# Kernel optimization log

Measured on AMD Instinct MI355X. Metric: run time of the kernel, lower is better.

Reference implementation:

```python
import jax, jax.numpy as jnp
import numpy as np

NUM_EXPERTS = 3
NUM_CLASSES = 10
HIDDEN = 256


def setup_inputs() -> dict:
    key = jax.random.key(0)
    k_in, k_w1, k_b1, k_w2, k_b2 = jax.random.split(key, 5)
    E, B, C, H, W = NUM_EXPERTS, 8, NUM_CLASSES, 512, 512
    inputs = jax.random.normal(k_in, (E, B, C, H, W), dtype=jnp.float32)
    fan_in1 = E * C
    w1 = jax.random.uniform(k_w1, (fan_in1, HIDDEN), jnp.float32, -1, 1) / np.sqrt(fan_in1)
    b1 = jax.random.uniform(k_b1, (HIDDEN,), jnp.float32, -1, 1) / np.sqrt(fan_in1)
    w2 = jax.random.uniform(k_w2, (HIDDEN, E), jnp.float32, -1, 1) / np.sqrt(HIDDEN)
    b2 = jax.random.uniform(k_b2, (E,), jnp.float32, -1, 1) / np.sqrt(HIDDEN)
    return {"inputs": inputs, "w1": w1, "b1": b1, "w2": w2, "b2": b2}


def reference(inputs, w1, b1, w2, b2):
    # inputs: [E, B, C, H, W] stacked expert logits
    E, B, C, H, W = inputs.shape
    N = B * H * W
    head_logits = jnp.moveaxis(inputs, 2, 1).reshape(E, C, N)   # [E, C, N]
    x = head_logits.reshape(E * C, N).T                          # [N, E*C]
    h = jax.nn.relu(x @ w1 + b1)                                 # [N, HIDDEN]
    exp_logits = h @ w2 + b2                                     # [N, E]
    # softmax is monotonic -> argmax of softmax == argmax of logits
    exp_selected = jnp.argmax(exp_logits, axis=-1)               # [N] int
    # gather the selected expert's logits per pixel (replaces one-hot mult-sum)
    out = head_logits[exp_selected, :, jnp.arange(N)]            # [N, C]
    output = out.T.reshape(C, B, H, W)                           # [C, B, H, W]
    output = jnp.moveaxis(output, 1, 0)                          # [B, C, H, W]
    return output, exp_selected.reshape(B, H, W)
```

## Files before the change

kernel.cpp:

```cpp
#include <hip/hip_runtime.h>

#define HWQ   262144
#define CHW   2621440
#define BCHW  20971520
#define NTOT  2097152

#define NBLOCKS 1024
#define BITERS  8

typedef __attribute__((ext_vector_type(8))) short short8;
typedef __attribute__((ext_vector_type(4))) float f32x4;

union Frag { uint u[4]; uint4 u4; short8 s; };

__device__ __forceinline__ uint bf16w(float x) {
    const uint u = __float_as_uint(x);
    return (u + 0x7FFFu + ((u >> 16) & 1u)) >> 16;
}

__device__ __forceinline__ void split_pair(float a, float b,
                                           uint& h, uint& m, uint& l) {
    const uint ha = bf16w(a), hb = bf16w(b);
    h = ha | (hb << 16);
    const float fa = __uint_as_float(ha << 16);
    const float fb = __uint_as_float(hb << 16);
    const float ra = a - fa, rb = b - fb;
    const uint ma = bf16w(ra), mb = bf16w(rb);
    m = ma | (mb << 16);
    const float ga = __uint_as_float(ma << 16);
    const float gb = __uint_as_float(mb << 16);
    l = bf16w(ra - ga) | (bf16w(rb - gb) << 16);
}

__global__ __launch_bounds__(512)
void mlp_select_mfma(const float* __restrict__ inputs,
                     const float* __restrict__ w1,
                     const float* __restrict__ b1,
                     const float* __restrict__ w2,
                     const float* __restrict__ b2,
                     float* __restrict__ out0,
                     float* __restrict__ out1) {
    __shared__ uint4 Bfrag[16 * 3 * 64];
    __shared__ float W2s[768];
    __shared__ float Logb[8 * 96];

    const int tid = threadIdx.x;

    for (int idx = tid; idx < 16 * 64; idx += 512) {
        const int ht = idx >> 6, ln = idx & 63;
        const int col = (ht << 4) | (ln & 15);
        const int kbs = (ln >> 4) << 3;
        Frag fh, fm, fl;
        #pragma unroll
        for (int jj = 0; jj < 4; ++jj) {
            const int k0 = kbs + 2 * jj, k1 = k0 + 1;
            const float a = (k0 < 30) ? w1[k0 * 256 + col]
                                      : ((k0 == 30) ? b1[col] : 0.f);
            const float b = (k1 < 30) ? w1[k1 * 256 + col]
                                      : ((k1 == 30) ? b1[col] : 0.f);
            split_pair(a, b, fh.u[jj], fm.u[jj], fl.u[jj]);
        }
        const int base = ht * 3 * 64 + ln;
        Bfrag[base]       = fh.u4;
        Bfrag[base + 64]  = fm.u4;
        Bfrag[base + 128] = fl.u4;
    }
    for (int i = tid; i < 768; i += 512) W2s[i] = w2[i];
    __syncthreads();

    const int lane = tid & 63;
    const int wid  = tid >> 6;
    const int l15  = lane & 15;
    const int lg   = lane >> 4;
    const int kb   = lg << 3;

    uint koff[8];
    #pragma unroll
    for (int j = 0; j < 8; ++j) {
        const int k = kb + j;
        const int e = (k >= 20) ? 2 : ((k >= 10) ? 1 : 0);
        const int c = k - e * 10;
        koff[j] = (k < 30) ? (uint)((e * BCHW + c * HWQ) * 4) : 0u;
    }
    const float b20 = b2[0], b21 = b2[1], b22 = b2[2];
    const char* ib = (const char*)inputs;
    char* ob = (char*)out0;

    #pragma unroll 1
    for (int it = 0; it < BITERS; ++it) {
        const int n0 = (blockIdx.x * BITERS + it) * 256 + wid * 32;
        const uint sbase = (uint)((n0 >> 18) * CHW + (n0 & (HWQ - 1))) * 4u;

        short8 Ah[2], Am[2], Al[2];
        #pragma unroll
        for (int t = 0; t < 2; ++t) {
            const uint vb = sbase + (uint)((t * 16 + l15) * 4);
            float xv[8];
            #pragma unroll
            for (int j = 0; j < 8; ++j)
                xv[j] = *(const float*)(ib + (size_t)(vb + koff[j]));
            if (kb == 24) { xv[6] = 1.f; xv[7] = 0.f; }
            Frag ch_, cm_, cl_;
            #pragma unroll
            for (int jj = 0; jj < 4; ++jj)
                split_pair(xv[2 * jj], xv[2 * jj + 1],
                           ch_.u[jj], cm_.u[jj], cl_.u[jj]);
            Ah[t] = ch_.s; Am[t] = cm_.s; Al[t] = cl_.s;
        }

        float lacc[2][4][3];
        #pragma unroll
        for (int t = 0; t < 2; ++t)
            #pragma unroll
            for (int r = 0; r < 4; ++r)
                lacc[t][r][0] = lacc[t][r][1] = lacc[t][r][2] = 0.f;

        #pragma unroll 4
        for (int ht = 0; ht < 16; ++ht) {
            const uint4* bp = &Bfrag[ht * 3 * 64 + lane];
            Frag bh, bm, bl;
            bh.u4 = bp[0]; bm.u4 = bp[64]; bl.u4 = bp[128];
            const int wcol = ((ht << 4) | l15) * 3;
            const float w20 = W2s[wcol], w21 = W2s[wcol + 1], w22 = W2s[wcol + 2];
            #pragma unroll
            for (int t = 0; t < 2; ++t) {
                f32x4 D = {0.f, 0.f, 0.f, 0.f};
                D = __builtin_amdgcn_mfma_f32_16x16x32_bf16(Al[t], bh.s, D, 0, 0, 0);
                D = __builtin_amdgcn_mfma_f32_16x16x32_bf16(Ah[t], bl.s, D, 0, 0, 0);
                D = __builtin_amdgcn_mfma_f32_16x16x32_bf16(Am[t], bm.s, D, 0, 0, 0);
                D = __builtin_amdgcn_mfma_f32_16x16x32_bf16(Am[t], bh.s, D, 0, 0, 0);
                D = __builtin_amdgcn_mfma_f32_16x16x32_bf16(Ah[t], bm.s, D, 0, 0, 0);
                D = __builtin_amdgcn_mfma_f32_16x16x32_bf16(Ah[t], bh.s, D, 0, 0, 0);
                #pragma unroll
                for (int r = 0; r < 4; ++r) {
                    const float hre = fmaxf(D[r], 0.f);
                    lacc[t][r][0] = fmaf(hre, w20, lacc[t][r][0]);
                    lacc[t][r][1] = fmaf(hre, w21, lacc[t][r][1]);
                    lacc[t][r][2] = fmaf(hre, w22, lacc[t][r][2]);
                }
            }
        }

        #pragma unroll
        for (int t = 0; t < 2; ++t)
            #pragma unroll
            for (int r = 0; r < 4; ++r)
                #pragma unroll
                for (int e = 0; e < 3; ++e) {
                    float v = lacc[t][r][e];
                    v += __shfl_xor(v, 1);
                    v += __shfl_xor(v, 2);
                    v += __shfl_xor(v, 4);
                    v += __shfl_xor(v, 8);
                    lacc[t][r][e] = v;
                }

        if (l15 == 0) {
            float* lb = &Logb[wid * 96];
            #pragma unroll
            for (int t = 0; t < 2; ++t)
                #pragma unroll
                for (int r = 0; r < 4; ++r) {
                    const int tk = t * 16 + lg * 4 + r;
                    lb[tk * 3 + 0] = lacc[t][r][0];
                    lb[tk * 3 + 1] = lacc[t][r][1];
                    lb[tk * 3 + 2] = lacc[t][r][2];
                }
        }
        __threadfence_block();

        const int tt = lane & 31;
        const float* lb = &Logb[wid * 96 + tt * 3];
        const float L0 = lb[0] + b20;
        const float L1 = lb[1] + b21;
        const float L2 = lb[2] + b22;
        int sel = 0; float best = L0;
        if (L1 > best) { best = L1; sel = 1; }
        if (L2 > best) { sel = 2; }

        const uint obase = sbase + (uint)(tt * 4);
        const uint ioff  = obase + (uint)sel * (uint)(BCHW * 4);
        const int chalf  = lane >> 5;
        #pragma unroll
        for (int cc = 0; cc < 5; ++cc) {
            const uint cofs = (uint)((chalf * 5 + cc) * (HWQ * 4));
            const float v = *(const float*)(ib + (size_t)(ioff + cofs));
            *(float*)(ob + (size_t)(obase + cofs)) = v;
        }
        if (lane < 32) out1[n0 + tt] = (float)sel;
    }
}

extern "C" void kernel_launch(void* const* d_in, const int* in_sizes, int n_in,
                              void* d_out, int out_size, void* d_ws, size_t ws_size,
                              hipStream_t stream) {
    const float* inputs = (const float*)d_in[0];
    const float* w1     = (const float*)d_in[1];
    const float* b1     = (const float*)d_in[2];
    const float* w2     = (const float*)d_in[3];
    const float* b2     = (const float*)d_in[4];

    float* out0 = (float*)d_out;
    float* out1 = out0 + BCHW;

    mlp_select_mfma<<<NBLOCKS, 512, 0, stream>>>(
        inputs, w1, b1, w2, b2, out0, out1);
}
```

Baseline: 496.4 us.

## Use persistent 768-block grid, occupancy hint, and shuffle-based argmax

Reduces the grid to 768 blocks that stride over 8192 work tiles, so each block handles about 11 tiles, and adds a launch-bounds occupancy hint of 6. The per-wave LDS logit buffer and its fence are replaced by computing the argmax in registers after the xor reduction, packing the selections into a word and redistributing it with a single shuffle. The b2 bias is folded into the accumulator initialisation, pre-scaled by 1/16 because the 16-lane reduction sums it back. The occupancy bound may force register spilling, and the last pass over the tiles leaves some blocks idle.

```diff
diff --git a/kernel.cpp b/kernel.cpp
--- a/kernel.cpp
+++ b/kernel.cpp
@@ -5,8 +5,9 @@
 #define BCHW  20971520
 #define NTOT  2097152
 
-#define NBLOCKS 1024
-#define BITERS  8
+#define NBLOCKS   768
+#define NBLKITER  8192
+#define BITERS    11
 
 typedef __attribute__((ext_vector_type(8))) short short8;
 typedef __attribute__((ext_vector_type(4))) float f32x4;
@@ -32,7 +33,7 @@
     l = bf16w(ra - ga) | (bf16w(rb - gb) << 16);
 }
 
-__global__ __launch_bounds__(512)
+__global__ __launch_bounds__(512, 6)
 void mlp_select_mfma(const float* __restrict__ inputs,
                      const float* __restrict__ w1,
                      const float* __restrict__ b1,
@@ -42,7 +43,6 @@
                      float* __restrict__ out1) {
     __shared__ uint4 Bfrag[16 * 3 * 64];
     __shared__ float W2s[768];
-    __shared__ float Logb[8 * 96];
 
     const int tid = threadIdx.x;
 
@@ -82,13 +82,15 @@
         const int c = k - e * 10;
         koff[j] = (k < 30) ? (uint)((e * BCHW + c * HWQ) * 4) : 0u;
     }
-    const float b20 = b2[0], b21 = b2[1], b22 = b2[2];
+    const float i20 = b2[0] * 0.0625f, i21 = b2[1] * 0.0625f, i22 = b2[2] * 0.0625f;
     const char* ib = (const char*)inputs;
     char* ob = (char*)out0;
 
     #pragma unroll 1
     for (int it = 0; it < BITERS; ++it) {
-        const int n0 = (blockIdx.x * BITERS + it) * 256 + wid * 32;
+        const int g = it * NBLOCKS + (int)blockIdx.x;
+        if (g >= NBLKITER) break;
+        const int n0 = g * 256 + wid * 32;
         const uint sbase = (uint)((n0 >> 18) * CHW + (n0 & (HWQ - 1))) * 4u;
 
         short8 Ah[2], Am[2], Al[2];
@@ -112,8 +114,9 @@
         #pragma unroll
         for (int t = 0; t < 2; ++t)
             #pragma unroll
-            for (int r = 0; r < 4; ++r)
-                lacc[t][r][0] = lacc[t][r][1] = lacc[t][r][2] = 0.f;
+            for (int r = 0; r < 4; ++r) {
+                lacc[t][r][0] = i20; lacc[t][r][1] = i21; lacc[t][r][2] = i22;
+            }
 
         #pragma unroll 4
         for (int ht = 0; ht < 16; ++ht) {
@@ -155,28 +158,24 @@
                     lacc[t][r][e] = v;
                 }
 
-        if (l15 == 0) {
-            float* lb = &Logb[wid * 96];
-            #pragma unroll
-            for (int t = 0; t < 2; ++t)
-                #pragma unroll
-                for (int r = 0; r < 4; ++r) {
-                    const int tk = t * 16 + lg * 4 + r;
-                    lb[tk * 3 + 0] = lacc[t][r][0];
-                    lb[tk * 3 + 1] = lacc[t][r][1];
-                    lb[tk * 3 + 2] = lacc[t][r][2];
-                }
-        }
-        __threadfence_block();
-
-        const int tt = lane & 31;
-        const float* lb = &Logb[wid * 96 + tt * 3];
-        const float L0 = lb[0] + b20;
-        const float L1 = lb[1] + b21;
-        const float L2 = lb[2] + b22;
-        int sel = 0; float best = L0;
-        if (L1 > best) { best = L1; sel = 1; }
-        if (L2 > best) { sel = 2; }
+        uint selpk = 0;
+        #pragma unroll
+        for (int t = 0; t < 2; ++t)
+            #pragma unroll
+            for (int r = 0; r < 4; ++r) {
+                const float L0 = lacc[t][r][0];
+                const float L1 = lacc[t][r][1];
+                const float L2 = lacc[t][r][2];
+                int sel = 0; float best = L0;
+                if (L1 > best) { best = L1; sel = 1; }
+                if (L2 > best) { sel = 2; }
+                selpk |= (uint)sel << ((t * 4 + r) * 2);
+            }
+
+        const int tt  = lane & 31;
+        const int src = (((tt >> 2) & 3) << 4) | l15;
+        const uint pk = (uint)__shfl((int)selpk, src);
+        const int sel = (int)((pk >> ((((tt >> 4) << 2) | (tt & 3)) * 2)) & 3u);
 
         const uint obase = sbase + (uint)(tt * 4);
         const uint ioff  = obase + (uint)sel * (uint)(BCHW * 4);
```

New measurement: 504.6 us. About the same (+1.7%).
